# Kernel optimization log

Hardware: AMD Instinct MI355X
Metric: run time of the kernel (lower is better)

The kernel has to match this reference:

```python
import jax, jax.numpy as jnp
import numpy as np

N_NODES = 10000
N_EDGES = 160000
IN_FEATS = 512
H_FEATS = 512
NUM_CLASSES = 128


def setup_inputs() -> dict:
    key = jax.random.key(0)
    ks = jax.random.split(key, 7)
    h = jax.random.normal(ks[0], (N_NODES, IN_FEATS), dtype=jnp.float32)
    W1 = jax.random.normal(ks[1], (2 * IN_FEATS, H_FEATS), dtype=jnp.float32) * 0.02
    b1 = jax.random.normal(ks[2], (H_FEATS,), dtype=jnp.float32) * 0.02
    W2 = jax.random.normal(ks[3], (2 * H_FEATS, NUM_CLASSES), dtype=jnp.float32) * 0.02
    b2 = jax.random.normal(ks[4], (NUM_CLASSES,), dtype=jnp.float32) * 0.02
    src = jax.random.randint(ks[5], (N_EDGES,), 0, N_NODES, dtype=jnp.int32)
    dst = jax.random.randint(ks[6], (N_EDGES,), 0, N_NODES, dtype=jnp.int32)
    return {"h": h, "W1": W1, "b1": b1, "W2": W2, "b2": b2, "src": src, "dst": dst}


def _weighted_sage_conv(h, W, b, src, dst, n_nodes):
    # message = u_mul_e('h','w') with w == ones -> just gather source features
    msg = h[src]  # [E, d]
    # fn.mean reduce at destination: segment-sum / in-degree (0 if no in-edges)
    s = jax.ops.segment_sum(msg, dst, num_segments=n_nodes)  # [N, d]
    cnt = jax.ops.segment_sum(jnp.ones((src.shape[0],), h.dtype), dst, num_segments=n_nodes)
    h_N = s / jnp.maximum(cnt, 1.0)[:, None]
    h_total = jnp.concatenate([h, h_N], axis=1)  # [N, 2d]
    return h_total @ W + b


def reference(h, W1, b1, W2, b2, src, dst):
    n = h.shape[0]
    h1 = jax.nn.relu(_weighted_sage_conv(h, W1, b1, src, dst, n))
    return _weighted_sage_conv(h1, W2, b2, src, dst, n)
```

## Files before the change

### kernel.cpp

```cpp
#include <hip/hip_runtime.h>

typedef unsigned short u16;
typedef unsigned char u8;
typedef __attribute__((ext_vector_type(2))) float floatx2;
typedef __attribute__((ext_vector_type(4))) float floatx4;
typedef __attribute__((ext_vector_type(8))) __bf16 bf16x8;
typedef __attribute__((ext_vector_type(2))) unsigned short us2;
typedef __attribute__((ext_vector_type(4))) unsigned short us4;
typedef __attribute__((ext_vector_type(8))) unsigned short us8;
typedef __attribute__((ext_vector_type(2))) unsigned int u32x2;

static __device__ __forceinline__ float b2f(u16 v) {
    union { unsigned u; float f; } x; x.u = ((unsigned)v) << 16; return x.f;
}
static __device__ __forceinline__ u16 f2b(float f) {
    union { float f; unsigned u; } x; x.f = f;
    unsigned u = x.u;
    return (u16)((u + 0x7fffu + ((u >> 16) & 1u)) >> 16);
}

#define GLOAD_LDS16(g, l) __builtin_amdgcn_global_load_lds( \
    (const __attribute__((address_space(1))) void*)(g),     \
    (__attribute__((address_space(3))) void*)(l), 16, 0, 0)

#define CAP 64
#define SPILLMAX 4096

static __device__ __forceinline__ int detect_blk(const u16* __restrict__ p,
                                                 int nelem, int* sh) {
    if (threadIdx.x == 0) *sh = 0;
    __syncthreads();
    const int lim = nelem < 512 ? nelem : 512;
    int found = 0;
    for (int j = threadIdx.x; 2 * j < lim; j += 256) {
        unsigned v = p[2 * j] & 0x7fffu;
        if (v >= 0x4280u) found = 1;
    }
    if (found) atomicOr(sh, 1);
    __syncthreads();
    return *sh;
}

static __device__ __forceinline__ int xcd_swz(int L, int nwg) {
    const int q = nwg >> 3, r = nwg & 7;
    const int x = L & 7, i = L >> 3;
    return (x < r ? x * (q + 1) : r * (q + 1) + (x - r) * q) + i;
}

__global__ __launch_bounds__(256) void k_d1(
    const int* __restrict__ src, const int* __restrict__ dst, int E, int Nn,
    int* __restrict__ cnt, int* __restrict__ bucket,
    int* __restrict__ nspill, int* __restrict__ spill,
    const void* __restrict__ h, const void* __restrict__ W1,
    const void* __restrict__ b1, const void* __restrict__ W2,
    const void* __restrict__ b2,
    u16* __restrict__ Hb, u16* __restrict__ W1T, u16* __restrict__ W2T,
    u16* __restrict__ b1c, u16* __restrict__ b2c, int* __restrict__ flags,
    int nFill, int nHb) {
    __shared__ u16 tile[32][33];
    __shared__ int sh;
    const int b = blockIdx.x;
    const int t = threadIdx.x;

    if (b < nFill) {
        int e = b * 256 + t;
        if (e < E) {
            int d = dst[e], s = src[e];
            if ((unsigned)d < (unsigned)Nn && (unsigned)s < (unsigned)Nn) {
                int p = atomicAdd(&cnt[d], 1);
                if (p < CAP) bucket[d * CAP + p] = s;
                else {
                    int q = atomicAdd(nspill, 1);
                    if (q < SPILLMAX) { spill[2 * q] = d; spill[2 * q + 1] = s; }
                }
            }
        }
        return;
    }
    if (b < nFill + nHb) {
        const int f = detect_blk((const u16*)h, Nn * 512, &sh);
        int i = ((b - nFill) * 256 + t) * 8;
        if (i >= Nn * 512) return;
        if (f) {
            const float* s = (const float*)h;
            us8 o;
#pragma unroll
            for (int k = 0; k < 8; ++k) o[k] = f2b(s[i + k]);
            *(us8*)(Hb + i) = o;
        } else {
            *(us8*)(Hb + i) = *(const us8*)((const u16*)h + i);
        }
        return;
    }
    if (b < nFill + nHb + 512) {
        const int f = detect_blk((const u16*)W1, 1024 * 512, &sh);
        int sub = b - nFill - nHb;
        int half = sub >> 8, idx = sub & 255;
        const int bx = (idx & 15) * 32, by = (idx >> 4) * 32;
        const int koff = half * 512, noff = half * 512;
        const int tx = t & 31, ty = t >> 5;
        for (int i = ty; i < 32; i += 8) {
            long id = (long)(koff + by + i) * 512 + (bx + tx);
            tile[i][tx] = f ? f2b(((const float*)W1)[id]) : ((const u16*)W1)[id];
        }
        __syncthreads();
        for (int i = ty; i < 32; i += 8)
            W1T[(long)(noff + bx + i) * 512 + (by + tx)] = tile[tx][i];
        return;
    }
    if (b < nFill + nHb + 640) {
        const int f = detect_blk((const u16*)W2, 1024 * 128, &sh);
        int sub = b - nFill - nHb - 512;
        int half = sub >> 6, idx = sub & 63;
        const int bx = (idx & 3) * 32, by = (idx >> 2) * 32;
        const int koff = half * 512, noff = half * 128;
        const int tx = t & 31, ty = t >> 5;
        for (int i = ty; i < 32; i += 8) {
            long id = (long)(koff + by + i) * 128 + (bx + tx);
            tile[i][tx] = f ? f2b(((const float*)W2)[id]) : ((const u16*)W2)[id];
        }
        __syncthreads();
        for (int i = ty; i < 32; i += 8)
            W2T[(long)(noff + bx + i) * 512 + (by + tx)] = tile[tx][i];
        return;
    }
    {
        const int f1 = detect_blk((const u16*)b1, 512, &sh);
        for (int i = t; i < 512; i += 256)
            b1c[i] = f1 ? f2b(((const float*)b1)[i]) : ((const u16*)b1)[i];
        const int f2 = detect_blk((const u16*)b2, 128, &sh);
        if (t < 128)
            b2c[t] = f2 ? f2b(((const float*)b2)[t]) : ((const u16*)b2)[t];
        const int fh = detect_blk((const u16*)h, Nn * 512, &sh);
        if (t == 0) flags[0] = fh;
    }
}

__device__ __forceinline__ void gemm_acc256(const u16* __restrict__ A,
                                            const u16* __restrict__ Bt,
                                            long brow, int bobs,
                                            floatx4 acc[4][4], u16* lA, u16* lB) {
    const int tid = threadIdx.x;
    const int wv = tid >> 6;
    const int ln = tid & 63;
    const int lrow = ln >> 2;
    const int lk = (ln & 3) * 8;
    const int m0 = ln & 15;
    const int kq = (ln >> 4) * 8;
    const int wc = wv * 64;

#pragma unroll
    for (int i = 0; i < 4; ++i)
#pragma unroll
        for (int j = 0; j < 4; ++j) acc[i][j] = (floatx4){0.f, 0.f, 0.f, 0.f};

    const u16* gA = A + (brow + wv * 16 + lrow) * 512 + lk;

    auto STAGE = [&](int kt, int sel) {
        u16* dA = lA + sel * 2048 + wv * 512;
        u16* dB = lB + sel * 8192;
        GLOAD_LDS16(gA + kt, dA);
#pragma unroll
        for (int ii = 0; ii < 4; ++ii) {
            const int c = ii * 4 + wv;
            GLOAD_LDS16(Bt + (long)(bobs + c * 16 + lrow) * 512 + kt + lk,
                        dB + c * 512);
        }
    };
    auto COMPUTE = [&](int sel) {
        const u16* rA = lA + sel * 2048;
        const u16* rB = lB + sel * 8192;
        bf16x8 af[4], bf[4];
#pragma unroll
        for (int i = 0; i < 4; ++i)
            af[i] = *(const bf16x8*)(rA + (i * 16 + m0) * 32 + kq);
#pragma unroll
        for (int j = 0; j < 4; ++j)
            bf[j] = *(const bf16x8*)(rB + (wc + j * 16 + m0) * 32 + kq);
#pragma unroll
        for (int i = 0; i < 4; ++i)
#pragma unroll
            for (int j = 0; j < 4; ++j)
                acc[i][j] = __builtin_amdgcn_mfma_f32_16x16x32_bf16(af[i], bf[j],
                                                                    acc[i][j], 0, 0, 0);
    };

    STAGE(0, 0);
    for (int t = 0; t < 15; ++t) {
        const int sel = t & 1;
        STAGE((t + 1) << 5, sel ^ 1);
        asm volatile("s_waitcnt vmcnt(5)" ::: "memory");
        __builtin_amdgcn_s_barrier();
        COMPUTE(sel);
        asm volatile("s_waitcnt lgkmcnt(0)" ::: "memory");
        __builtin_amdgcn_s_barrier();
    }
    asm volatile("s_waitcnt vmcnt(0)" ::: "memory");
    __builtin_amdgcn_s_barrier();
    COMPUTE(1);
}

__global__ __launch_bounds__(256) void k_gemm1_256(
    const u16* __restrict__ A, const u16* __restrict__ Bt,
    u16* __restrict__ C1s, u8* __restrict__ P1, int Mstore) {
    __shared__ __align__(16) u16 lA[2 * 64 * 32];
    __shared__ __align__(16) u16 lB[2 * 256 * 32];
    const int L = blockIdx.y * gridDim.x + blockIdx.x;
    const int T = xcd_swz(L, gridDim.x * gridDim.y);
    const int by = T & 3;
    const int bcol = by * 256;
    const long brow = (long)(T >> 2) * 64;
    floatx4 acc[4][4];
    gemm_acc256(A, Bt, brow, bcol, acc, lA, lB);

    const int ln = threadIdx.x & 63;
    const int wv = threadIdx.x >> 6;
    const int wc = wv * 64;
    const int m0 = ln & 15;
    const int q4 = (ln >> 4) * 4;
    if (by < 2) {
#pragma unroll
        for (int i = 0; i < 4; ++i)
#pragma unroll
            for (int r = 0; r < 4; ++r) {
                long row = brow + i * 16 + q4 + r;
                if (row < Mstore) {
#pragma unroll
                    for (int j = 0; j < 4; ++j)
                        C1s[row * 512 + (bcol + wc + j * 16 + m0)] = f2b(acc[i][j][r]);
                }
            }
    } else {
        const int coff = bcol - 512;
#pragma unroll
        for (int i = 0; i < 4; ++i)
#pragma unroll
            for (int r = 0; r < 4; ++r) {
                long row = brow + i * 16 + q4 + r;
                if (row < Mstore) {
#pragma unroll
                    for (int j = 0; j < 4; ++j) {
                        float v = acc[i][j][r];
                        int pk = __builtin_amdgcn_cvt_pk_fp8_f32(v, v, 0, false);
                        P1[row * 512 + (coff + wc + j * 16 + m0)] = (u8)(pk & 0xff);
                    }
                }
            }
    }
}

__device__ __forceinline__ void gemm_acc64(const u16* __restrict__ A,
                                           const u16* __restrict__ Bt,
                                           long brow, int bobs,
                                           floatx4 acc[4][2], u16* lA, u16* lB) {
    const int tid = threadIdx.x;
    const int wv = tid >> 6;
    const int ln = tid & 63;
    const int lrow = ln >> 2;
    const int lk = (ln & 3) * 8;
    const int m0 = ln & 15;
    const int kq = (ln >> 4) * 8;
    const int wc = wv * 32;

#pragma unroll
    for (int i = 0; i < 4; ++i)
#pragma unroll
        for (int j = 0; j < 2; ++j) acc[i][j] = (floatx4){0.f, 0.f, 0.f, 0.f};

    const u16* gA = A + (brow + wv * 16 + lrow) * 512 + lk;

    auto STAGE = [&](int kt, int sel) {
        u16* dA = lA + sel * 2048 + wv * 512;
        u16* dB = lB + sel * 4096;
        GLOAD_LDS16(gA + kt, dA);
#pragma unroll
        for (int ii = 0; ii < 2; ++ii) {
            const int c = ii * 4 + wv;
            GLOAD_LDS16(Bt + (long)(bobs + c * 16 + lrow) * 512 + kt + lk,
                        dB + c * 512);
        }
    };
    auto COMPUTE = [&](int sel) {
        const u16* rA = lA + sel * 2048;
        const u16* rB = lB + sel * 4096;
        bf16x8 af[4], bf[2];
#pragma unroll
        for (int i = 0; i < 4; ++i)
            af[i] = *(const bf16x8*)(rA + (i * 16 + m0) * 32 + kq);
#pragma unroll
        for (int j = 0; j < 2; ++j)
            bf[j] = *(const bf16x8*)(rB + (wc + j * 16 + m0) * 32 + kq);
#pragma unroll
        for (int i = 0; i < 4; ++i)
#pragma unroll
            for (int j = 0; j < 2; ++j)
                acc[i][j] = __builtin_amdgcn_mfma_f32_16x16x32_bf16(af[i], bf[j],
                                                                    acc[i][j], 0, 0, 0);
    };

    STAGE(0, 0);
    for (int t = 0; t < 15; ++t) {
        const int sel = t & 1;
        STAGE((t + 1) << 5, sel ^ 1);
        asm volatile("s_waitcnt vmcnt(3)" ::: "memory");
        __builtin_amdgcn_s_barrier();
        COMPUTE(sel);
        asm volatile("s_waitcnt lgkmcnt(0)" ::: "memory");
        __builtin_amdgcn_s_barrier();
    }
    asm volatile("s_waitcnt vmcnt(0)" ::: "memory");
    __builtin_amdgcn_s_barrier();
    COMPUTE(1);
}

__global__ __launch_bounds__(256) void k_gemm2_64(
    const u16* __restrict__ A, const u16* __restrict__ Bt,
    u16* __restrict__ C2s, u16* __restrict__ P2, int Mstore) {
    __shared__ __align__(16) u16 lA[2 * 64 * 32];
    __shared__ __align__(16) u16 lB[2 * 128 * 32];
    const int L = blockIdx.y * gridDim.x + blockIdx.x;
    const int T = xcd_swz(L, gridDim.x * gridDim.y);
    const int by = T & 1;
    const long brow = (long)(T >> 1) * 64;
    floatx4 acc[4][2];
    gemm_acc64(A, Bt, brow, by * 128, acc, lA, lB);

    u16* C = by ? P2 : C2s;
    const int ln = threadIdx.x & 63;
    const int wv = threadIdx.x >> 6;
    const int wc = wv * 32;
    const int m0 = ln & 15;
    const int q4 = (ln >> 4) * 4;
#pragma unroll
    for (int i = 0; i < 4; ++i)
#pragma unroll
        for (int r = 0; r < 4; ++r) {
            long row = brow + i * 16 + q4 + r;
            if (row < Mstore) {
#pragma unroll
                for (int j = 0; j < 2; ++j)
                    C[row * 128 + (wc + j * 16 + m0)] = f2b(acc[i][j][r]);
            }
        }
}

__global__ __launch_bounds__(256) void agg_h1(const u8* __restrict__ P1,
                                              const u16* __restrict__ C1s,
                                              const u16* __restrict__ b1c,
                                              const int* __restrict__ cnt,
                                              const int* __restrict__ bucket,
                                              const int* __restrict__ nspill,
                                              const int* __restrict__ spill,
                                              u16* __restrict__ h1, int Nn) {
    const int n = blockIdx.x * 4 + (threadIdx.x >> 6);
    const int l = threadIdx.x & 63;
    if (n >= Nn) return;
    const int c = cnt[n];
    const int inb = c < CAP ? c : CAP;
    const int* bk = bucket + (long)n * CAP;
    float a0 = 0.f, a1 = 0.f, a2 = 0.f, a3 = 0.f;
    float a4 = 0.f, a5 = 0.f, a6 = 0.f, a7 = 0.f;
    int e = 0;
    for (; e + 7 < inb; e += 8) {
        u32x2 w[8];
#pragma unroll
        for (int q = 0; q < 8; ++q) {
            int s = bk[e + q];
            w[q] = *(const u32x2*)(P1 + (long)s * 512 + l * 8);
        }
#pragma unroll
        for (int q = 0; q < 8; ++q) {
            floatx2 f0 = __builtin_amdgcn_cvt_pk_f32_fp8(w[q][0], false);
            floatx2 f1 = __builtin_amdgcn_cvt_pk_f32_fp8(w[q][0], true);
            floatx2 f2 = __builtin_amdgcn_cvt_pk_f32_fp8(w[q][1], false);
            floatx2 f3 = __builtin_amdgcn_cvt_pk_f32_fp8(w[q][1], true);
            a0 += f0[0]; a1 += f0[1]; a2 += f1[0]; a3 += f1[1];
            a4 += f2[0]; a5 += f2[1]; a6 += f3[0]; a7 += f3[1];
        }
    }
    for (; e + 3 < inb; e += 4) {
        u32x2 w[4];
#pragma unroll
        for (int q = 0; q < 4; ++q) {
            int s = bk[e + q];
            w[q] = *(const u32x2*)(P1 + (long)s * 512 + l * 8);
        }
#pragma unroll
        for (int q = 0; q < 4; ++q) {
            floatx2 f0 = __builtin_amdgcn_cvt_pk_f32_fp8(w[q][0], false);
            floatx2 f1 = __builtin_amdgcn_cvt_pk_f32_fp8(w[q][0], true);
            floatx2 f2 = __builtin_amdgcn_cvt_pk_f32_fp8(w[q][1], false);
            floatx2 f3 = __builtin_amdgcn_cvt_pk_f32_fp8(w[q][1], true);
            a0 += f0[0]; a1 += f0[1]; a2 += f1[0]; a3 += f1[1];
            a4 += f2[0]; a5 += f2[1]; a6 += f3[0]; a7 += f3[1];
        }
    }
    for (; e < inb; ++e) {
        int s = bk[e];
        u32x2 w = *(const u32x2*)(P1 + (long)s * 512 + l * 8);
        floatx2 f0 = __builtin_amdgcn_cvt_pk_f32_fp8(w[0], false);
        floatx2 f1 = __builtin_amdgcn_cvt_pk_f32_fp8(w[0], true);
        floatx2 f2 = __builtin_amdgcn_cvt_pk_f32_fp8(w[1], false);
        floatx2 f3 = __builtin_amdgcn_cvt_pk_f32_fp8(w[1], true);
        a0 += f0[0]; a1 += f0[1]; a2 += f1[0]; a3 += f1[1];
        a4 += f2[0]; a5 += f2[1]; a6 += f3[0]; a7 += f3[1];
    }
    const int ns = *nspill;
    if (ns > 0) {
        int lim = ns < SPILLMAX ? ns : SPILLMAX;
        for (int q = 0; q < lim; ++q) {
            if (spill[2 * q] == n) {
                int s = spill[2 * q + 1];
                u32x2 w = *(const u32x2*)(P1 + (long)s * 512 + l * 8);
                floatx2 f0 = __builtin_amdgcn_cvt_pk_f32_fp8(w[0], false);
                floatx2 f1 = __builtin_amdgcn_cvt_pk_f32_fp8(w[0], true);
                floatx2 f2 = __builtin_amdgcn_cvt_pk_f32_fp8(w[1], false);
                floatx2 f3 = __builtin_amdgcn_cvt_pk_f32_fp8(w[1], true);
                a0 += f0[0]; a1 += f0[1]; a2 += f1[0]; a3 += f1[1];
                a4 += f2[0]; a5 += f2[1]; a6 += f3[0]; a7 += f3[1];
            }
        }
    }
    float inv = 1.0f / (float)(c > 1 ? c : 1);
    us8 sf = *(const us8*)(C1s + (long)n * 512 + l * 8);
    us8 bv = *(const us8*)(b1c + l * 8);
    us8 o;
    o[0] = f2b(fmaxf(b2f(sf[0]) + a0 * inv + b2f(bv[0]), 0.f));
    o[1] = f2b(fmaxf(b2f(sf[1]) + a1 * inv + b2f(bv[1]), 0.f));
    o[2] = f2b(fmaxf(b2f(sf[2]) + a2 * inv + b2f(bv[2]), 0.f));
    o[3] = f2b(fmaxf(b2f(sf[3]) + a3 * inv + b2f(bv[3]), 0.f));
    o[4] = f2b(fmaxf(b2f(sf[4]) + a4 * inv + b2f(bv[4]), 0.f));
    o[5] = f2b(fmaxf(b2f(sf[5]) + a5 * inv + b2f(bv[5]), 0.f));
    o[6] = f2b(fmaxf(b2f(sf[6]) + a6 * inv + b2f(bv[6]), 0.f));
    o[7] = f2b(fmaxf(b2f(sf[7]) + a7 * inv + b2f(bv[7]), 0.f));
    *(us8*)(h1 + (long)n * 512 + l * 8) = o;
}

__global__ __launch_bounds__(256) void agg_out(const u16* __restrict__ P2,
                                               const u16* __restrict__ C2s,
                                               const u16* __restrict__ b2c,
                                               const int* __restrict__ cnt,
                                               const int* __restrict__ bucket,
                                               const int* __restrict__ nspill,
                                               const int* __restrict__ spill,
                                               void* __restrict__ outv, int Nn,
                                               const int* __restrict__ flags) {
    const int n = blockIdx.x * 4 + (threadIdx.x >> 6);
    const int l = threadIdx.x & 63;
    if (n >= Nn) return;
    const int c = cnt[n];
    const int inb = c < CAP ? c : CAP;
    const int* bk = bucket + (long)n * CAP;
    float a0 = 0.f, a1 = 0.f;
    int e = 0;
    for (; e + 3 < inb; e += 4) {
        int s0 = bk[e], s1 = bk[e + 1], s2 = bk[e + 2], s3 = bk[e + 3];
        us2 v0 = *(const us2*)(P2 + (long)s0 * 128 + l * 2);
        us2 v1 = *(const us2*)(P2 + (long)s1 * 128 + l * 2);
        us2 v2 = *(const us2*)(P2 + (long)s2 * 128 + l * 2);
        us2 v3 = *(const us2*)(P2 + (long)s3 * 128 + l * 2);
        a0 += (b2f(v0[0]) + b2f(v1[0])) + (b2f(v2[0]) + b2f(v3[0]));
        a1 += (b2f(v0[1]) + b2f(v1[1])) + (b2f(v2[1]) + b2f(v3[1]));
    }
    for (; e < inb; ++e) {
        int s0 = bk[e];
        us2 v0 = *(const us2*)(P2 + (long)s0 * 128 + l * 2);
        a0 += b2f(v0[0]); a1 += b2f(v0[1]);
    }
    const int ns = *nspill;
    if (ns > 0) {
        int lim = ns < SPILLMAX ? ns : SPILLMAX;
        for (int q = 0; q < lim; ++q) {
            if (spill[2 * q] == n) {
                int s0 = spill[2 * q + 1];
                us2 v0 = *(const us2*)(P2 + (long)s0 * 128 + l * 2);
                a0 += b2f(v0[0]); a1 += b2f(v0[1]);
            }
        }
    }
    float inv = 1.0f / (float)(c > 1 ? c : 1);
    us2 sf = *(const us2*)(C2s + (long)n * 128 + l * 2);
    us2 bv = *(const us2*)(b2c + l * 2);
    float o0 = b2f(sf[0]) + a0 * inv + b2f(bv[0]);
    float o1 = b2f(sf[1]) + a1 * inv + b2f(bv[1]);
    if (flags[0]) {
        float* o = (float*)outv + (long)n * 128 + l * 2;
        o[0] = o0; o[1] = o1;
    } else {
        us2 ob; ob[0] = f2b(o0); ob[1] = f2b(o1);
        *(us2*)((u16*)outv + (long)n * 128 + l * 2) = ob;
    }
}

extern "C" void kernel_launch(void* const* d_in, const int* in_sizes, int n_in,
                              void* d_out, int out_size, void* d_ws, size_t ws_size,
                              hipStream_t stream) {
    const int D = 512, NCLS = 128;
    const int Nn = in_sizes[0] / D;
    const int E  = in_sizes[5];
    const int mtiles = (Nn + 127) / 128;
    const int mt64 = (Nn + 63) / 64;
    const int Mpad = mtiles * 128;
    const int nFill = (E + 255) / 256;
    const int nHb = (Nn * D / 8 + 255) / 256;

    const int* src = (const int*)d_in[5];
    const int* dst = (const int*)d_in[6];

    char* p = (char*)d_ws;
    u16* Hb  = (u16*)p; p += (size_t)Mpad * D * 2;
    u16* h1  = (u16*)p; p += (size_t)Mpad * D * 2;
    u16* C1s = (u16*)p; p += (size_t)Mpad * D * 2;
    u8*  P1  = (u8*)p;  p += (size_t)Mpad * D;
    u16* C2s = (u16*)p; p += (size_t)Mpad * NCLS * 2;
    u16* P2  = (u16*)p; p += (size_t)Mpad * NCLS * 2;
    u16* W1T = (u16*)p; p += (size_t)1024 * D * 2;
    u16* W2T = (u16*)p; p += (size_t)256 * D * 2;
    u16* b1c = (u16*)p; p += 1024;
    u16* b2c = (u16*)p; p += 1024;
    int* flags  = (int*)p; p += 256;
    int* cnt    = (int*)p; p += (size_t)(Nn + 60) * 4;
    int* nspill = cnt + Nn;
    int* bucket = (int*)p; p += (size_t)Nn * CAP * 4;
    int* spill  = (int*)p; p += (size_t)SPILLMAX * 2 * 4;

    hipMemsetAsync(cnt, 0, (size_t)(Nn + 60) * 4, stream);

    k_d1<<<nFill + nHb + 641, 256, 0, stream>>>(
        src, dst, E, Nn, cnt, bucket, nspill, spill,
        d_in[0], d_in[1], d_in[2], d_in[3], d_in[4],
        Hb, W1T, W2T, b1c, b2c, flags, nFill, nHb);

    k_gemm1_256<<<dim3(mt64, 4), 256, 0, stream>>>(Hb, W1T, C1s, P1, Nn);

    agg_h1<<<(Nn + 3) / 4, 256, 0, stream>>>(P1, C1s, b1c, cnt, bucket,
                                             nspill, spill, h1, Nn);

    k_gemm2_64<<<dim3(mt64, 2), 256, 0, stream>>>(h1, W2T, C2s, P2, Nn);

    agg_out<<<(Nn + 3) / 4, 256, 0, stream>>>(P2, C2s, b2c, cnt, bucket,
                                              nspill, spill, d_out, Nn, flags);
}
```

Baseline: 149.0 us.

## Retile GEMM1 to 128x128 with 2x2 waves and triple-buffer both GEMMs

GEMM1 moves from 64x256 block tiles to 128x128 tiles, with the four waves arranged 2x2 so each computes a 64x64 sub-tile. This balances A and B loads per block and doubles the rows handled per block. Both GEMM kernels switch from double- to triple-buffered LDS staging, with waitcnt thresholds adjusted so loads run two k-steps ahead. The cost is more LDS per block, which may lower occupancy, and it relies on mtiles being defined for 128-row tiles.

Measured after the change: 148.1 us. No clear change (-0.5%).

```diff
diff --git a/kernel.cpp b/kernel.cpp
--- a/kernel.cpp
+++ b/kernel.cpp
@@ -136,7 +136,7 @@
     }
 }
 
-__device__ __forceinline__ void gemm_acc256(const u16* __restrict__ A,
+__device__ __forceinline__ void gemm_acc128(const u16* __restrict__ A,
                                             const u16* __restrict__ Bt,
                                             long brow, int bobs,
                                             floatx4 acc[4][4], u16* lA, u16* lB) {
@@ -147,33 +147,32 @@
     const int lk = (ln & 3) * 8;
     const int m0 = ln & 15;
     const int kq = (ln >> 4) * 8;
-    const int wc = wv * 64;
+    const int wr = (wv >> 1) * 64;
+    const int wc = (wv & 1) * 64;
 
 #pragma unroll
     for (int i = 0; i < 4; ++i)
 #pragma unroll
         for (int j = 0; j < 4; ++j) acc[i][j] = (floatx4){0.f, 0.f, 0.f, 0.f};
 
-    const u16* gA = A + (brow + wv * 16 + lrow) * 512 + lk;
-
     auto STAGE = [&](int kt, int sel) {
-        u16* dA = lA + sel * 2048 + wv * 512;
-        u16* dB = lB + sel * 8192;
-        GLOAD_LDS16(gA + kt, dA);
-#pragma unroll
-        for (int ii = 0; ii < 4; ++ii) {
+        u16* dA = lA + sel * 4096;
+        u16* dB = lB + sel * 4096;
+#pragma unroll
+        for (int ii = 0; ii < 2; ++ii) {
             const int c = ii * 4 + wv;
+            GLOAD_LDS16(A + (brow + c * 16 + lrow) * 512 + kt + lk, dA + c * 512);
             GLOAD_LDS16(Bt + (long)(bobs + c * 16 + lrow) * 512 + kt + lk,
                         dB + c * 512);
         }
     };
     auto COMPUTE = [&](int sel) {
-        const u16* rA = lA + sel * 2048;
-        const u16* rB = lB + sel * 8192;
+        const u16* rA = lA + sel * 4096;
+        const u16* rB = lB + sel * 4096;
         bf16x8 af[4], bf[4];
 #pragma unroll
         for (int i = 0; i < 4; ++i)
-            af[i] = *(const bf16x8*)(rA + (i * 16 + m0) * 32 + kq);
+            af[i] = *(const bf16x8*)(rA + (wr + i * 16 + m0) * 32 + kq);
 #pragma unroll
         for (int j = 0; j < 4; ++j)
             bf[j] = *(const bf16x8*)(rB + (wc + j * 16 + m0) * 32 + kq);
@@ -186,44 +185,52 @@
     };
 
     STAGE(0, 0);
-    for (int t = 0; t < 15; ++t) {
-        const int sel = t & 1;
-        STAGE((t + 1) << 5, sel ^ 1);
-        asm volatile("s_waitcnt vmcnt(5)" ::: "memory");
+    STAGE(32, 1);
+    int cur = 0, nxt = 1, fut = 2;
+    for (int t = 0; t < 14; ++t) {
+        STAGE((t + 2) << 5, fut);
+        asm volatile("s_waitcnt vmcnt(8)" ::: "memory");
         __builtin_amdgcn_s_barrier();
-        COMPUTE(sel);
+        COMPUTE(cur);
         asm volatile("s_waitcnt lgkmcnt(0)" ::: "memory");
         __builtin_amdgcn_s_barrier();
-    }
+        int tmp = cur; cur = nxt; nxt = fut; fut = tmp;
+    }
+    asm volatile("s_waitcnt vmcnt(4)" ::: "memory");
+    __builtin_amdgcn_s_barrier();
+    COMPUTE(cur);
+    asm volatile("s_waitcnt lgkmcnt(0)" ::: "memory");
+    __builtin_amdgcn_s_barrier();
     asm volatile("s_waitcnt vmcnt(0)" ::: "memory");
     __builtin_amdgcn_s_barrier();
-    COMPUTE(1);
-}
-
-__global__ __launch_bounds__(256) void k_gemm1_256(
+    COMPUTE(nxt);
+}
+
+__global__ __launch_bounds__(256) void k_gemm1_128(
     const u16* __restrict__ A, const u16* __restrict__ Bt,
     u16* __restrict__ C1s, u8* __restrict__ P1, int Mstore) {
-    __shared__ __align__(16) u16 lA[2 * 64 * 32];
-    __shared__ __align__(16) u16 lB[2 * 256 * 32];
+    __shared__ __align__(16) u16 lA[3 * 128 * 32];
+    __shared__ __align__(16) u16 lB[3 * 128 * 32];
     const int L = blockIdx.y * gridDim.x + blockIdx.x;
     const int T = xcd_swz(L, gridDim.x * gridDim.y);
-    const int by = T & 3;
-    const int bcol = by * 256;
-    const long brow = (long)(T >> 2) * 64;
+    const int by = T & 7;
+    const int bcol = by * 128;
+    const long brow = (long)(T >> 3) * 128;
     floatx4 acc[4][4];
-    gemm_acc256(A, Bt, brow, bcol, acc, lA, lB);
+    gemm_acc128(A, Bt, brow, bcol, acc, lA, lB);
 
     const int ln = threadIdx.x & 63;
     const int wv = threadIdx.x >> 6;
-    const int wc = wv * 64;
+    const int wr = (wv >> 1) * 64;
+    const int wc = (wv & 1) * 64;
     const int m0 = ln & 15;
     const int q4 = (ln >> 4) * 4;
-    if (by < 2) {
+    if (by < 4) {
 #pragma unroll
         for (int i = 0; i < 4; ++i)
 #pragma unroll
             for (int r = 0; r < 4; ++r) {
-                long row = brow + i * 16 + q4 + r;
+                long row = brow + wr + i * 16 + q4 + r;
                 if (row < Mstore) {
 #pragma unroll
                     for (int j = 0; j < 4; ++j)
@@ -236,7 +243,7 @@
         for (int i = 0; i < 4; ++i)
 #pragma unroll
             for (int r = 0; r < 4; ++r) {
-                long row = brow + i * 16 + q4 + r;
+                long row = brow + wr + i * 16 + q4 + r;
                 if (row < Mstore) {
 #pragma unroll
                     for (int j = 0; j < 4; ++j) {
@@ -299,25 +306,32 @@
     };
 
     STAGE(0, 0);
-    for (int t = 0; t < 15; ++t) {
-        const int sel = t & 1;
-        STAGE((t + 1) << 5, sel ^ 1);
-        asm volatile("s_waitcnt vmcnt(3)" ::: "memory");
+    STAGE(32, 1);
+    int cur = 0, nxt = 1, fut = 2;
+    for (int t = 0; t < 14; ++t) {
+        STAGE((t + 2) << 5, fut);
+        asm volatile("s_waitcnt vmcnt(6)" ::: "memory");
         __builtin_amdgcn_s_barrier();
-        COMPUTE(sel);
+        COMPUTE(cur);
         asm volatile("s_waitcnt lgkmcnt(0)" ::: "memory");
         __builtin_amdgcn_s_barrier();
-    }
+        int tmp = cur; cur = nxt; nxt = fut; fut = tmp;
+    }
+    asm volatile("s_waitcnt vmcnt(3)" ::: "memory");
+    __builtin_amdgcn_s_barrier();
+    COMPUTE(cur);
+    asm volatile("s_waitcnt lgkmcnt(0)" ::: "memory");
+    __builtin_amdgcn_s_barrier();
     asm volatile("s_waitcnt vmcnt(0)" ::: "memory");
     __builtin_amdgcn_s_barrier();
-    COMPUTE(1);
+    COMPUTE(nxt);
 }
 
 __global__ __launch_bounds__(256) void k_gemm2_64(
     const u16* __restrict__ A, const u16* __restrict__ Bt,
     u16* __restrict__ C2s, u16* __restrict__ P2, int Mstore) {
-    __shared__ __align__(16) u16 lA[2 * 64 * 32];
-    __shared__ __align__(16) u16 lB[2 * 128 * 32];
+    __shared__ __align__(16) u16 lA[3 * 64 * 32];
+    __shared__ __align__(16) u16 lB[3 * 128 * 32];
     const int L = blockIdx.y * gridDim.x + blockIdx.x;
     const int T = xcd_swz(L, gridDim.x * gridDim.y);
     const int by = T & 1;
@@ -531,7 +545,7 @@
         d_in[0], d_in[1], d_in[2], d_in[3], d_in[4],
         Hb, W1T, W2T, b1c, b2c, flags, nFill, nHb);
 
-    k_gemm1_256<<<dim3(mt64, 4), 256, 0, stream>>>(Hb, W1T, C1s, P1, Nn);
+    k_gemm1_128<<<dim3(mtiles, 8), 256, 0, stream>>>(Hb, W1T, C1s, P1, Nn);
 
     agg_h1<<<(Nn + 3) / 4, 256, 0, stream>>>(P1, C1s, b1c, cnt, bucket,
                                              nspill, spill, h1, Nn);
```
